# Optimization experiments

Hardware: AMD Instinct MI355X
Metric: run time of the kernel (lower is better)

## Reference

```python
import jax, jax.numpy as jnp
import numpy as np

N_NODES = 20000
N_EDGES = 240000
IN_DIM = 20
SH_DIM = 16  # (lmax+1)^2 with lmax=3
DENOM = 1.0
EPS = 1e-12


def spherical_harmonics_lmax3(v):
    """Real spherical harmonics l=0..3 on unit vectors v: [E,3] -> [E,16]."""
    x, y, z = v[:, 0], v[:, 1], v[:, 2]
    x2, y2, z2 = x * x, y * y, z * z
    sh = [
        jnp.full_like(x, 0.28209479177387814),            # l=0
        0.4886025119029199 * y,                            # l=1, m=-1
        0.4886025119029199 * z,                            # l=1, m=0
        0.4886025119029199 * x,                            # l=1, m=1
        1.0925484305920792 * x * y,                        # l=2, m=-2
        1.0925484305920792 * y * z,                        # l=2, m=-1
        0.31539156525252005 * (3.0 * z2 - 1.0),            # l=2, m=0
        1.0925484305920792 * x * z,                        # l=2, m=1
        0.5462742152960396 * (x2 - y2),                    # l=2, m=2
        0.5900435899266435 * y * (3.0 * x2 - y2),          # l=3, m=-3
        2.890611442640554 * x * y * z,                     # l=3, m=-2
        0.4570457994644658 * y * (5.0 * z2 - 1.0),         # l=3, m=-1
        0.3731763325901154 * z * (5.0 * z2 - 3.0),         # l=3, m=0
        0.4570457994644658 * x * (5.0 * z2 - 1.0),         # l=3, m=1
        1.445305721320277 * z * (x2 - y2),                 # l=3, m=2
        0.5900435899266435 * x * (x2 - 3.0 * y2),          # l=3, m=3
    ]
    return jnp.stack(sh, axis=-1)


def setup_inputs() -> dict:
    key = jax.random.key(0)
    ks = jax.random.split(key, 10)
    x = jax.random.normal(ks[0], (N_NODES, IN_DIM), dtype=jnp.float32)
    positions = jax.random.normal(ks[1], (N_NODES, 3), dtype=jnp.float32)
    edge_index = jax.random.randint(ks[2], (2, N_EDGES), 0, N_NODES, dtype=jnp.int32)
    s = 1.0 / np.sqrt(IN_DIM)
    W_pre = jax.random.uniform(ks[3], (IN_DIM, IN_DIM), jnp.float32, -s, s)
    b_pre = jax.random.uniform(ks[4], (IN_DIM,), jnp.float32, -s, s)
    W_post = jax.random.uniform(ks[5], (IN_DIM, IN_DIM), jnp.float32, -s, s)
    b_post = jax.random.uniform(ks[6], (IN_DIM,), jnp.float32, -s, s)
    W_sc = jax.random.uniform(ks[7], (IN_DIM, IN_DIM), jnp.float32, -s, s)
    b_sc = jax.random.uniform(ks[8], (IN_DIM,), jnp.float32, -s, s)
    return {"x": x, "positions": positions, "edge_index": edge_index,
            "W_pre": W_pre, "b_pre": b_pre, "W_post": W_post, "b_post": b_post,
            "W_sc": W_sc, "b_sc": b_sc}


def reference(x, positions, edge_index, W_pre, b_pre, W_post, b_post, W_sc, b_sc):
    row, col = edge_index[0], edge_index[1]
    # per-edge gather + relative positions
    rel = positions[col] - positions[row]                      # [E,3]
    norm = jnp.sqrt(jnp.sum(rel * rel, axis=-1, keepdims=True) + EPS)
    sh = spherical_harmonics_lmax3(rel / norm)                 # [E,16]
    sender = x[row]                                            # [E,20]
    # equivariant tensor product (outer product over irreps channels)
    tp = (sender[:, :, None] * sh[:, None, :]).reshape(sender.shape[0], IN_DIM * SH_DIM)  # [E,320]
    edge_features = jnp.concatenate([sender, tp], axis=1)      # [E,340]
    # scatter-add aggregation to target nodes
    aggr = jax.ops.segment_sum(edge_features, col, num_segments=N_NODES)  # [N,340]
    # node update MLP + shortcut (math of Layer.update)
    h = x / DENOM
    h = jax.nn.relu(h @ W_pre.T + b_pre)
    h = h @ W_post.T + b_post
    out = x @ W_sc.T + b_sc + h                                # [N,20]
    # aggr is computed (and aggregated) by the original propagate; concat so it stays live
    return jnp.concatenate([out, aggr], axis=1)                # [N,360]
```

## Files before the change

### kernel.cpp

```cpp
#include <hip/hip_runtime.h>

#define N_NODES 20000
#define N_EDGES 240000
#define IN_DIM  20
#define AGG_DIM 340
#define OUT_DIM 360
#define EPS_F   1e-12f
#define CAP     32
#define POISON  ((int)0xAAAAAAAA)
#define EDGE_BLOCKS ((N_EDGES + 255) / 256)
#define MLP_BLOCKS  ((N_NODES + 255) / 256)

typedef _Float16 half8 __attribute__((ext_vector_type(8)));

__device__ __forceinline__ float sh_coeff(int k, float xn, float yn, float zn) {
    const float x2 = xn * xn, y2 = yn * yn, z2 = zn * zn;
    switch (k) {
        case 0:  return 0.28209479177387814f;
        case 1:  return 0.4886025119029199f * yn;
        case 2:  return 0.4886025119029199f * zn;
        case 3:  return 0.4886025119029199f * xn;
        case 4:  return 1.0925484305920792f * xn * yn;
        case 5:  return 1.0925484305920792f * yn * zn;
        case 6:  return 0.31539156525252005f * (3.0f * z2 - 1.0f);
        case 7:  return 1.0925484305920792f * xn * zn;
        case 8:  return 0.5462742152960396f * (x2 - y2);
        case 9:  return 0.5900435899266435f * yn * (3.0f * x2 - y2);
        case 10: return 2.890611442640554f  * xn * yn * zn;
        case 11: return 0.4570457994644658f * yn * (5.0f * z2 - 1.0f);
        case 12: return 0.3731763325901154f * zn * (5.0f * z2 - 3.0f);
        case 13: return 0.4570457994644658f * xn * (5.0f * z2 - 1.0f);
        case 14: return 1.445305721320277f  * zn * (x2 - y2);
        default: return 0.5900435899266435f * xn * (x2 - 3.0f * y2);
    }
}

__global__ __launch_bounds__(256) void bucket_sh_mlp(
    const float* __restrict__ pos,
    const int* __restrict__ ei,
    const float* __restrict__ x,
    const float* __restrict__ Wpre,  const float* __restrict__ bpre,
    const float* __restrict__ Wpost, const float* __restrict__ bpost,
    const float* __restrict__ Wsc,   const float* __restrict__ bsc,
    int* __restrict__ counts,
    int* __restrict__ ovf_cnt,
    int* __restrict__ ovf,
    int* __restrict__ bucket,
    _Float16* __restrict__ shbuf,
    float* __restrict__ out)
{
    if ((int)blockIdx.x < EDGE_BLOCKS) {
        const int e = (int)(blockIdx.x * 256 + threadIdx.x);
        if (e >= N_EDGES) return;
        const int row = ei[e];
        const int col = ei[N_EDGES + e];

        atomicCAS(&counts[col], POISON, 0);
        const int slot = atomicAdd(&counts[col], 1);
        if (slot >= CAP) {
            atomicCAS(ovf_cnt, POISON, 0);
            ovf[atomicAdd(ovf_cnt, 1)] = e;
            return;
        }

        const int sidx = col * CAP + slot;
        bucket[sidx] = row;

        const float rx = pos[col * 3 + 0] - pos[row * 3 + 0];
        const float ry = pos[col * 3 + 1] - pos[row * 3 + 1];
        const float rz = pos[col * 3 + 2] - pos[row * 3 + 2];
        const float rinv = rsqrtf(rx * rx + ry * ry + rz * rz + EPS_F);
        const float xx = rx * rinv, yy = ry * rinv, zz = rz * rinv;
        const float x2 = xx * xx, y2 = yy * yy, z2 = zz * zz;

        const float sh0  = 0.28209479177387814f;
        const float sh1  = 0.4886025119029199f * yy;
        const float sh2  = 0.4886025119029199f * zz;
        const float sh3  = 0.4886025119029199f * xx;
        const float sh4  = 1.0925484305920792f * xx * yy;
        const float sh5  = 1.0925484305920792f * yy * zz;
        const float sh6  = 0.31539156525252005f * (3.0f * z2 - 1.0f);
        const float sh7  = 1.0925484305920792f * xx * zz;
        const float sh8  = 0.5462742152960396f * (x2 - y2);
        const float sh9  = 0.5900435899266435f * yy * (3.0f * x2 - y2);
        const float sh10 = 2.890611442640554f  * xx * yy * zz;
        const float sh11 = 0.4570457994644658f * yy * (5.0f * z2 - 1.0f);
        const float sh12 = 0.3731763325901154f * zz * (5.0f * z2 - 3.0f);
        const float sh13 = 0.4570457994644658f * xx * (5.0f * z2 - 1.0f);
        const float sh14 = 1.445305721320277f  * zz * (x2 - y2);
        const float sh15 = 0.5900435899266435f * xx * (x2 - 3.0f * y2);

        const half8 v0 = { (_Float16)sh12, (_Float16)sh13, (_Float16)sh14, (_Float16)sh15,
                           (_Float16)sh0,  (_Float16)sh1,  (_Float16)sh2,  (_Float16)sh3 };
        const half8 v1 = { (_Float16)sh4,  (_Float16)sh5,  (_Float16)sh6,  (_Float16)sh7,
                           (_Float16)sh8,  (_Float16)sh9,  (_Float16)sh10, (_Float16)sh11 };
        half8* dst = (half8*)(shbuf + (size_t)sidx * 16);
        dst[0] = v0;
        dst[1] = v1;
        return;
    }

    __shared__ float sWpre[IN_DIM * IN_DIM];
    __shared__ float sWpost[IN_DIM * IN_DIM];
    __shared__ float sWsc[IN_DIM * IN_DIM];
    __shared__ float sb[3 * IN_DIM];

    for (int t = (int)threadIdx.x; t < IN_DIM * IN_DIM; t += 256) {
        sWpre[t]  = Wpre[t];
        sWpost[t] = Wpost[t];
        sWsc[t]   = Wsc[t];
    }
    if (threadIdx.x < IN_DIM) {
        sb[threadIdx.x]              = bpre[threadIdx.x];
        sb[IN_DIM + threadIdx.x]     = bpost[threadIdx.x];
        sb[2 * IN_DIM + threadIdx.x] = bsc[threadIdx.x];
    }
    __syncthreads();

    const int i = (int)((blockIdx.x - EDGE_BLOCKS) * 256 + threadIdx.x);
    if (i >= N_NODES) return;

    float xi[IN_DIM], h[IN_DIM];
#pragma unroll
    for (int j = 0; j < IN_DIM; ++j) xi[j] = x[(size_t)i * IN_DIM + j];
#pragma unroll
    for (int j = 0; j < IN_DIM; ++j) {
        float a = sb[j];
#pragma unroll
        for (int kk = 0; kk < IN_DIM; ++kk) a = fmaf(xi[kk], sWpre[j * IN_DIM + kk], a);
        h[j] = fmaxf(a, 0.0f);
    }
#pragma unroll
    for (int j = 0; j < IN_DIM; ++j) {
        float a = sb[IN_DIM + j] + sb[2 * IN_DIM + j];
#pragma unroll
        for (int kk = 0; kk < IN_DIM; ++kk) {
            a = fmaf(h[kk],  sWpost[j * IN_DIM + kk], a);
            a = fmaf(xi[kk], sWsc[j * IN_DIM + kk],  a);
        }
        out[(size_t)i * OUT_DIM + j] = a;
    }
}

__global__ __launch_bounds__(256) void node_gather(
    const float* __restrict__ x,
    const float* __restrict__ pos,
    const int* __restrict__ ei,
    const int* __restrict__ counts,
    const int* __restrict__ bucket,
    const _Float16* __restrict__ shbuf,
    const int* __restrict__ ovf_cnt,
    const int* __restrict__ ovf,
    float* __restrict__ out)
{
    const int lane   = (int)(threadIdx.x & 63);
    const int node   = (int)((blockIdx.x * blockDim.x + threadIdx.x) >> 6);
    const int lane20 = min(lane, IN_DIM - 1);
    const int lane16 = lane & 15;

    const int j0 = (lane >= IN_DIM) ? ((lane - IN_DIM) >> 4) : 0;
    const int j1 = (lane + 44)  >> 4;
    const int j2 = (lane + 108) >> 4;
    const int j3 = (lane + 172) >> 4;
    const int j4 = (lane + 236) >> 4;
    const int j5 = (lane + 300) >> 4;

    const int cnt_raw = __builtin_amdgcn_readfirstlane(counts[node]);
    const int cnt = min(cnt_raw, CAP);

    float acc0 = 0.f, acc1 = 0.f, acc2 = 0.f, acc3 = 0.f, acc4 = 0.f, acc5 = 0.f;
    float sum_s = 0.f;

#define ACCUM(S, SH)                                      \
    do {                                                  \
        sum_s += (S);                                     \
        acc0 = fmaf(__shfl((S), j0, 64), (SH), acc0);     \
        acc1 = fmaf(__shfl((S), j1, 64), (SH), acc1);     \
        acc2 = fmaf(__shfl((S), j2, 64), (SH), acc2);     \
        acc3 = fmaf(__shfl((S), j3, 64), (SH), acc3);     \
        acc4 = fmaf(__shfl((S), j4, 64), (SH), acc4);     \
        acc5 = fmaf(__shfl((S), j5, 64), (SH), acc5);     \
    } while (0)

    if (cnt > 0) {
        const int rl = bucket[node * CAP + min(lane, cnt - 1)];
        const _Float16* shb = shbuf + (size_t)node * CAP * 16 + lane16;

        for (int base = 0; base < cnt; base += 4) {
            const int q1 = min(base + 1, cnt - 1);
            const int q2 = min(base + 2, cnt - 1);
            const int q3 = min(base + 3, cnt - 1);
            const int r0 = __builtin_amdgcn_readlane(rl, base);
            const int r1 = __builtin_amdgcn_readlane(rl, q1);
            const int r2 = __builtin_amdgcn_readlane(rl, q2);
            const int r3 = __builtin_amdgcn_readlane(rl, q3);

            const float sA = x[(size_t)r0 * IN_DIM + lane20];
            float       sB = x[(size_t)r1 * IN_DIM + lane20];
            float       sC = x[(size_t)r2 * IN_DIM + lane20];
            float       sD = x[(size_t)r3 * IN_DIM + lane20];
            const float shA = (float)shb[(size_t)base * 16];
            const float shB = (float)shb[(size_t)q1 * 16];
            const float shC = (float)shb[(size_t)q2 * 16];
            const float shD = (float)shb[(size_t)q3 * 16];

            sB = (base + 1 < cnt) ? sB : 0.0f;
            sC = (base + 2 < cnt) ? sC : 0.0f;
            sD = (base + 3 < cnt) ? sD : 0.0f;

            ACCUM(sA, shA);
            ACCUM(sB, shB);
            ACCUM(sC, shC);
            ACCUM(sD, shD);
        }
    }

    if (cnt_raw > CAP) {
        const int m = *ovf_cnt;
        const int k = (lane + 12) & 15;
        for (int i = 0; i < m; ++i) {
            const int e = ovf[i];
            if (ei[N_EDGES + e] != node) continue;
            const int row = ei[e];
            const float rx = pos[node * 3 + 0] - pos[row * 3 + 0];
            const float ry = pos[node * 3 + 1] - pos[row * 3 + 1];
            const float rz = pos[node * 3 + 2] - pos[row * 3 + 2];
            const float rinv = rsqrtf(rx * rx + ry * ry + rz * rz + EPS_F);
            const float shk = sh_coeff(k, rx * rinv, ry * rinv, rz * rinv);
            const float s = x[(size_t)row * IN_DIM + lane20];
            ACCUM(s, shk);
        }
    }
#undef ACCUM

    float* obase = out + (size_t)node * OUT_DIM + IN_DIM;
    obase[lane]       = (lane < IN_DIM) ? sum_s : acc0;
    obase[lane + 64]  = acc1;
    obase[lane + 128] = acc2;
    obase[lane + 192] = acc3;
    obase[lane + 256] = acc4;
    if (lane < IN_DIM) obase[lane + 320] = acc5;
}

extern "C" void kernel_launch(void* const* d_in, const int* in_sizes, int n_in,
                              void* d_out, int out_size, void* d_ws, size_t ws_size,
                              hipStream_t stream)
{
    const float* x     = (const float*)d_in[0];
    const float* pos   = (const float*)d_in[1];
    const int*   ei    = (const int*)d_in[2];
    const float* Wpre  = (const float*)d_in[3];
    const float* bpre  = (const float*)d_in[4];
    const float* Wpost = (const float*)d_in[5];
    const float* bpost = (const float*)d_in[6];
    const float* Wsc   = (const float*)d_in[7];
    const float* bsc   = (const float*)d_in[8];
    float* out = (float*)d_out;

    _Float16* shbuf = (_Float16*)d_ws;
    int* ws_i    = (int*)((char*)d_ws + (size_t)N_NODES * CAP * 16 * sizeof(_Float16));
    int* counts  = ws_i;
    int* ovf_cnt = ws_i + N_NODES;
    int* ovf     = ws_i + N_NODES + 1;
    int* bucket  = ws_i + N_NODES + 1 + N_EDGES;

    bucket_sh_mlp<<<EDGE_BLOCKS + MLP_BLOCKS, 256, 0, stream>>>(
        pos, ei, x, Wpre, bpre, Wpost, bpost, Wsc, bsc,
        counts, ovf_cnt, ovf, bucket, shbuf, out);

    node_gather<<<(N_NODES * 64) / 256, 256, 0, stream>>>(
        x, pos, ei, counts, bucket, shbuf, ovf_cnt, ovf, out);
}
```

Baseline: 133.3 us.

## Compute spherical harmonics in gather kernel via LDS instead of global fp16 buffer

Moves the spherical harmonics computation out of the edge-bucketing pass and into the per-node gather kernel. Each lane computes the 16 coefficients for one incoming edge and writes them to a padded shared-memory tile, which removes the global fp16 SH buffer write and its later read. The POISON-based counter initialisation is replaced by an explicit memset of the counters before launch. The cost is an extra block-wide barrier and per-node position gathers in the gather kernel, plus one more launch for the memset; SH values are now kept in fp32.

```diff
diff --git a/kernel.cpp b/kernel.cpp
--- a/kernel.cpp
+++ b/kernel.cpp
@@ -7,11 +7,9 @@
 #define OUT_DIM 360
 #define EPS_F   1e-12f
 #define CAP     32
-#define POISON  ((int)0xAAAAAAAA)
+#define SH_LD   17
 #define EDGE_BLOCKS ((N_EDGES + 255) / 256)
 #define MLP_BLOCKS  ((N_NODES + 255) / 256)
-
-typedef _Float16 half8 __attribute__((ext_vector_type(8)));
 
 __device__ __forceinline__ float sh_coeff(int k, float xn, float yn, float zn) {
     const float x2 = xn * xn, y2 = yn * yn, z2 = zn * zn;
@@ -35,8 +33,7 @@
     }
 }
 
-__global__ __launch_bounds__(256) void bucket_sh_mlp(
-    const float* __restrict__ pos,
+__global__ __launch_bounds__(256) void bucket_mlp(
     const int* __restrict__ ei,
     const float* __restrict__ x,
     const float* __restrict__ Wpre,  const float* __restrict__ bpre,
@@ -46,7 +43,6 @@
     int* __restrict__ ovf_cnt,
     int* __restrict__ ovf,
     int* __restrict__ bucket,
-    _Float16* __restrict__ shbuf,
     float* __restrict__ out)
 {
     if ((int)blockIdx.x < EDGE_BLOCKS) {
@@ -54,49 +50,9 @@
         if (e >= N_EDGES) return;
         const int row = ei[e];
         const int col = ei[N_EDGES + e];
-
-        atomicCAS(&counts[col], POISON, 0);
         const int slot = atomicAdd(&counts[col], 1);
-        if (slot >= CAP) {
-            atomicCAS(ovf_cnt, POISON, 0);
-            ovf[atomicAdd(ovf_cnt, 1)] = e;
-            return;
-        }
-
-        const int sidx = col * CAP + slot;
-        bucket[sidx] = row;
-
-        const float rx = pos[col * 3 + 0] - pos[row * 3 + 0];
-        const float ry = pos[col * 3 + 1] - pos[row * 3 + 1];
-        const float rz = pos[col * 3 + 2] - pos[row * 3 + 2];
-        const float rinv = rsqrtf(rx * rx + ry * ry + rz * rz + EPS_F);
-        const float xx = rx * rinv, yy = ry * rinv, zz = rz * rinv;
-        const float x2 = xx * xx, y2 = yy * yy, z2 = zz * zz;
-
-        const float sh0  = 0.28209479177387814f;
-        const float sh1  = 0.4886025119029199f * yy;
-        const float sh2  = 0.4886025119029199f * zz;
-        const float sh3  = 0.4886025119029199f * xx;
-        const float sh4  = 1.0925484305920792f * xx * yy;
-        const float sh5  = 1.0925484305920792f * yy * zz;
-        const float sh6  = 0.31539156525252005f * (3.0f * z2 - 1.0f);
-        const float sh7  = 1.0925484305920792f * xx * zz;
-        const float sh8  = 0.5462742152960396f * (x2 - y2);
-        const float sh9  = 0.5900435899266435f * yy * (3.0f * x2 - y2);
-        const float sh10 = 2.890611442640554f  * xx * yy * zz;
-        const float sh11 = 0.4570457994644658f * yy * (5.0f * z2 - 1.0f);
-        const float sh12 = 0.3731763325901154f * zz * (5.0f * z2 - 3.0f);
-        const float sh13 = 0.4570457994644658f * xx * (5.0f * z2 - 1.0f);
-        const float sh14 = 1.445305721320277f  * zz * (x2 - y2);
-        const float sh15 = 0.5900435899266435f * xx * (x2 - 3.0f * y2);
-
-        const half8 v0 = { (_Float16)sh12, (_Float16)sh13, (_Float16)sh14, (_Float16)sh15,
-                           (_Float16)sh0,  (_Float16)sh1,  (_Float16)sh2,  (_Float16)sh3 };
-        const half8 v1 = { (_Float16)sh4,  (_Float16)sh5,  (_Float16)sh6,  (_Float16)sh7,
-                           (_Float16)sh8,  (_Float16)sh9,  (_Float16)sh10, (_Float16)sh11 };
-        half8* dst = (half8*)(shbuf + (size_t)sidx * 16);
-        dst[0] = v0;
-        dst[1] = v1;
+        if (slot < CAP) bucket[col * CAP + slot] = row;
+        else            ovf[atomicAdd(ovf_cnt, 1)] = e;
         return;
     }
 
@@ -148,15 +104,51 @@
     const int* __restrict__ ei,
     const int* __restrict__ counts,
     const int* __restrict__ bucket,
-    const _Float16* __restrict__ shbuf,
     const int* __restrict__ ovf_cnt,
     const int* __restrict__ ovf,
     float* __restrict__ out)
 {
+    __shared__ float shl[4][CAP * SH_LD];
+
     const int lane   = (int)(threadIdx.x & 63);
+    const int wid    = (int)(threadIdx.x >> 6);
     const int node   = (int)((blockIdx.x * blockDim.x + threadIdx.x) >> 6);
     const int lane20 = min(lane, IN_DIM - 1);
-    const int lane16 = lane & 15;
+
+    const int cnt_raw = __builtin_amdgcn_readfirstlane(counts[node]);
+    const int cnt = min(cnt_raw, CAP);
+
+    const int rl = bucket[node * CAP + min(lane, cnt - 1)];
+
+    float* myshl = shl[wid];
+    if (lane < cnt) {
+        const int row = rl;
+        const float rx = pos[node * 3 + 0] - pos[row * 3 + 0];
+        const float ry = pos[node * 3 + 1] - pos[row * 3 + 1];
+        const float rz = pos[node * 3 + 2] - pos[row * 3 + 2];
+        const float rinv = rsqrtf(rx * rx + ry * ry + rz * rz + EPS_F);
+        const float xx = rx * rinv, yy = ry * rinv, zz = rz * rinv;
+        const float x2 = xx * xx, y2 = yy * yy, z2 = zz * zz;
+
+        float* d = myshl + lane * SH_LD;
+        d[0]  = 0.28209479177387814f;
+        d[1]  = 0.4886025119029199f * yy;
+        d[2]  = 0.4886025119029199f * zz;
+        d[3]  = 0.4886025119029199f * xx;
+        d[4]  = 1.0925484305920792f * xx * yy;
+        d[5]  = 1.0925484305920792f * yy * zz;
+        d[6]  = 0.31539156525252005f * (3.0f * z2 - 1.0f);
+        d[7]  = 1.0925484305920792f * xx * zz;
+        d[8]  = 0.5462742152960396f * (x2 - y2);
+        d[9]  = 0.5900435899266435f * yy * (3.0f * x2 - y2);
+        d[10] = 2.890611442640554f  * xx * yy * zz;
+        d[11] = 0.4570457994644658f * yy * (5.0f * z2 - 1.0f);
+        d[12] = 0.3731763325901154f * zz * (5.0f * z2 - 3.0f);
+        d[13] = 0.4570457994644658f * xx * (5.0f * z2 - 1.0f);
+        d[14] = 1.445305721320277f  * zz * (x2 - y2);
+        d[15] = 0.5900435899266435f * xx * (x2 - 3.0f * y2);
+    }
+    __syncthreads();
 
     const int j0 = (lane >= IN_DIM) ? ((lane - IN_DIM) >> 4) : 0;
     const int j1 = (lane + 44)  >> 4;
@@ -164,9 +156,7 @@
     const int j3 = (lane + 172) >> 4;
     const int j4 = (lane + 236) >> 4;
     const int j5 = (lane + 300) >> 4;
-
-    const int cnt_raw = __builtin_amdgcn_readfirstlane(counts[node]);
-    const int cnt = min(cnt_raw, CAP);
+    const int kL = (lane + 12) & 15;
 
     float acc0 = 0.f, acc1 = 0.f, acc2 = 0.f, acc3 = 0.f, acc4 = 0.f, acc5 = 0.f;
     float sum_s = 0.f;
@@ -183,8 +173,7 @@
     } while (0)
 
     if (cnt > 0) {
-        const int rl = bucket[node * CAP + min(lane, cnt - 1)];
-        const _Float16* shb = shbuf + (size_t)node * CAP * 16 + lane16;
+        const float* shb = myshl + kL;
 
         for (int base = 0; base < cnt; base += 4) {
             const int q1 = min(base + 1, cnt - 1);
@@ -199,10 +188,10 @@
             float       sB = x[(size_t)r1 * IN_DIM + lane20];
             float       sC = x[(size_t)r2 * IN_DIM + lane20];
             float       sD = x[(size_t)r3 * IN_DIM + lane20];
-            const float shA = (float)shb[(size_t)base * 16];
-            const float shB = (float)shb[(size_t)q1 * 16];
-            const float shC = (float)shb[(size_t)q2 * 16];
-            const float shD = (float)shb[(size_t)q3 * 16];
+            const float shA = shb[base * SH_LD];
+            const float shB = shb[q1 * SH_LD];
+            const float shC = shb[q2 * SH_LD];
+            const float shD = shb[q3 * SH_LD];
 
             sB = (base + 1 < cnt) ? sB : 0.0f;
             sC = (base + 2 < cnt) ? sC : 0.0f;
@@ -217,7 +206,6 @@
 
     if (cnt_raw > CAP) {
         const int m = *ovf_cnt;
-        const int k = (lane + 12) & 15;
         for (int i = 0; i < m; ++i) {
             const int e = ovf[i];
             if (ei[N_EDGES + e] != node) continue;
@@ -226,7 +214,7 @@
             const float ry = pos[node * 3 + 1] - pos[row * 3 + 1];
             const float rz = pos[node * 3 + 2] - pos[row * 3 + 2];
             const float rinv = rsqrtf(rx * rx + ry * ry + rz * rz + EPS_F);
-            const float shk = sh_coeff(k, rx * rinv, ry * rinv, rz * rinv);
+            const float shk = sh_coeff(kL, rx * rinv, ry * rinv, rz * rinv);
             const float s = x[(size_t)row * IN_DIM + lane20];
             ACCUM(s, shk);
         }
@@ -257,17 +245,18 @@
     const float* bsc   = (const float*)d_in[8];
     float* out = (float*)d_out;
 
-    _Float16* shbuf = (_Float16*)d_ws;
-    int* ws_i    = (int*)((char*)d_ws + (size_t)N_NODES * CAP * 16 * sizeof(_Float16));
+    int* ws_i    = (int*)d_ws;
     int* counts  = ws_i;
     int* ovf_cnt = ws_i + N_NODES;
     int* ovf     = ws_i + N_NODES + 1;
     int* bucket  = ws_i + N_NODES + 1 + N_EDGES;
 
-    bucket_sh_mlp<<<EDGE_BLOCKS + MLP_BLOCKS, 256, 0, stream>>>(
-        pos, ei, x, Wpre, bpre, Wpost, bpost, Wsc, bsc,
-        counts, ovf_cnt, ovf, bucket, shbuf, out);
+    hipMemsetAsync(counts, 0, (size_t)(N_NODES + 1) * sizeof(int), stream);
+
+    bucket_mlp<<<EDGE_BLOCKS + MLP_BLOCKS, 256, 0, stream>>>(
+        ei, x, Wpre, bpre, Wpost, bpost, Wsc, bsc,
+        counts, ovf_cnt, ovf, bucket, out);
 
     node_gather<<<(N_NODES * 64) / 256, 256, 0, stream>>>(
-        x, pos, ei, counts, bucket, shbuf, ovf_cnt, ovf, out);
-}
+        x, pos, ei, counts, bucket, ovf_cnt, ovf, out);
+}
```

Result: faster. 127.8 us (-4.2%).
